# Performance work log

Hardware: AMD Instinct MI355X
Metric: run time of the kernel (lower is better)

The kernel has to match this reference:

```python
import jax, jax.numpy as jnp
import numpy as np

N_NODES = 100000
N_EDGES = 1600000
HEADS = 8
CH = 16
NEG_SLOPE = 0.2


def setup_inputs() -> dict:
    key = jax.random.key(0)
    ks = jax.random.split(key, 8)
    x = jax.random.normal(ks[0], (N_NODES, 16), dtype=jnp.float32)
    edge_index = jax.random.randint(ks[1], (2, N_EDGES), 0, N_NODES, dtype=jnp.int64)
    W = jax.random.normal(ks[2], (16, HEADS * CH), dtype=jnp.float32) * 0.25
    att_src = jax.random.normal(ks[3], (HEADS, CH), dtype=jnp.float32) * 0.25
    att_dst = jax.random.normal(ks[4], (HEADS, CH), dtype=jnp.float32) * 0.25
    bias = jax.random.normal(ks[5], (HEADS * CH,), dtype=jnp.float32) * 0.1
    fc_w = jax.random.normal(ks[6], (HEADS * CH, 5), dtype=jnp.float32) * 0.1
    fc_b = jax.random.normal(ks[7], (5,), dtype=jnp.float32) * 0.1
    return {"x": x, "edge_index": edge_index, "W": W, "att_src": att_src,
            "att_dst": att_dst, "bias": bias, "fc_w": fc_w, "fc_b": fc_b}


def reference(x, edge_index, W, att_src, att_dst, bias, fc_w, fc_b):
    N = x.shape[0]
    # PyG GATConv default: add self loops
    loops = jnp.arange(N, dtype=edge_index.dtype)
    src = jnp.concatenate([edge_index[0], loops])
    dst = jnp.concatenate([edge_index[1], loops])

    h = (x @ W).reshape(N, HEADS, CH)                 # [N,H,C]
    a_src = jnp.einsum('nhc,hc->nh', h, att_src)      # [N,H]
    a_dst = jnp.einsum('nhc,hc->nh', h, att_dst)      # [N,H]

    e = a_src[src] + a_dst[dst]                       # [E,H]
    e = jax.nn.leaky_relu(e, NEG_SLOPE)
    # segment softmax over edges grouped by destination node
    e_max = jax.ops.segment_max(e, dst, num_segments=N)
    e_exp = jnp.exp(e - e_max[dst])
    denom = jax.ops.segment_sum(e_exp, dst, num_segments=N)
    alpha = e_exp / (denom[dst] + 1e-16)              # [E,H]

    msg = alpha[:, :, None] * h[src]                  # [E,H,C]
    out = jax.ops.segment_sum(msg, dst, num_segments=N)  # [N,H,C]
    out = out.reshape(N, HEADS * CH) + bias           # concat heads + bias

    out = jax.nn.relu(out)
    # dropout is identity in eval mode
    logits = out @ fc_w + fc_b                        # [N,5]
    return jax.nn.log_softmax(logits, axis=1)
```

## Files before the change

### kernel.cpp

```cpp
#include <hip/hip_runtime.h>
#include <hip/hip_bf16.h>
#include <math.h>

#define N_NODES 100000
#define N_EDGES 1600000
#define HEADS 8
#define HC 128
#define LOG2E 1.44269504f

#define DPB 64
#define NB 1563
#define NBP (NB + 1)
#define NCH 512
#define EPC (N_EDGES / NCH)
#define CAPS 2048
#define NA 196

__global__ __launch_bounds__(512) void k_prep(
    const float* __restrict__ x, const float* __restrict__ W,
    const float* __restrict__ att_s, const float* __restrict__ att_d,
    const int* __restrict__ ei,
    unsigned short* __restrict__ a_srcb, float* __restrict__ a_dst,
    uint4* __restrict__ x2b,
    int* __restrict__ offs, unsigned* __restrict__ stg) {
    __shared__ int smem[2048 + EPC];
    __shared__ int ws8[8];
    int t = threadIdx.x;
    if (blockIdx.x >= NCH) {
        float* sM = (float*)smem;
        if (t < 256) {
            int k = t >> 4, h2 = t & 15;
            const float* av = (h2 < 8) ? att_s : att_d;
            int h = h2 & 7;
            float s = 0.f;
#pragma unroll
            for (int c = 0; c < 16; ++c)
                s = fmaf(W[k * HC + h * 16 + c], av[h * 16 + c], s);
            sM[k * 16 + h2] = s * LOG2E;
        }
        __syncthreads();
        int node = (blockIdx.x - NCH) * 512 + t;
        if (node < N_NODES) {
            const float4* xr = (const float4*)(x + node * 16);
            float4 x0 = xr[0], x1 = xr[1], x2 = xr[2], x3 = xr[3];
            float xv[16] = {x0.x, x0.y, x0.z, x0.w, x1.x, x1.y, x1.z, x1.w,
                            x2.x, x2.y, x2.z, x2.w, x3.x, x3.y, x3.z, x3.w};
            union { uint4 u[2]; __hip_bfloat162 b[8]; } px;
#pragma unroll
            for (int k = 0; k < 8; ++k)
                px.b[k] = __float22bfloat162_rn(float2{xv[2 * k], xv[2 * k + 1]});
            x2b[node * 2] = px.u[0];
            x2b[node * 2 + 1] = px.u[1];
#pragma unroll
            for (int h2 = 0; h2 < 16; ++h2) {
                float o = 0.f;
#pragma unroll
                for (int k = 0; k < 16; ++k) o = fmaf(xv[k], sM[k * 16 + h2], o);
                if (h2 < 8) a_srcb[node * 8 + h2] =
                    __bfloat16_as_ushort(__float2bfloat16(o));
                else        a_dst[node * 8 + (h2 - 8)] = o;
            }
        }
    } else {
        int* hist = smem;
        unsigned* entries = (unsigned*)(smem + 2048);
        int c = blockIdx.x;
        hist[t] = 0; hist[t + 512] = 0; hist[t + 1024] = 0; hist[t + 1536] = 0;
        __syncthreads();
        int beg = c * EPC, end = beg + EPC;
        for (int e = beg + t; e < end; e += 512)
            atomicAdd(&hist[ei[N_EDGES + e] >> 6], 1);
        __syncthreads();
        int i0 = 4 * t;
        int v0 = hist[i0], v1 = hist[i0 + 1], v2 = hist[i0 + 2], v3 = hist[i0 + 3];
        int s1 = v0 + v1, s2 = s1 + v2, T = s2 + v3;
        int lane = t & 63, wv = t >> 6;
        int inc = T;
#pragma unroll
        for (int off = 1; off < 64; off <<= 1) {
            int y = __shfl_up(inc, off);
            if (lane >= off) inc += y;
        }
        if (lane == 63) ws8[wv] = inc;
        __syncthreads();
        int wbase = 0;
        for (int k = 0; k < wv; ++k) wbase += ws8[k];
        int e0 = wbase + inc - T;
        hist[i0] = e0; hist[i0 + 1] = e0 + v0;
        hist[i0 + 2] = e0 + s1; hist[i0 + 3] = e0 + s2;
        __syncthreads();
        int row = c * NBP;
        for (int b = t; b < NB; b += 512) offs[row + b] = hist[b];
        if (t == 0) offs[row + NB] = EPC;
        __syncthreads();
        for (int e = beg + t; e < end; e += 512) {
            int src = ei[e], dst = ei[N_EDGES + e];
            int pos = atomicAdd(&hist[dst >> 6], 1);
            entries[pos] = ((unsigned)(dst & 63) << 17) | (unsigned)src;
        }
        __syncthreads();
        unsigned* so = stg + beg;
        for (int i = t; i < EPC; i += 512) so[i] = entries[i];
    }
}

__global__ __launch_bounds__(256) void k_tr(const int* __restrict__ offs,
                                            int* __restrict__ offsT) {
    __shared__ int tile[64][65];
    int b0 = (blockIdx.x >> 3) * 64;
    int c0 = (blockIdx.x & 7) * 64;
    int t = threadIdx.x;
    for (int i = t; i < 4096; i += 256) {
        int cc = i >> 6, bb = i & 63;
        int b = b0 + bb;
        tile[bb][cc] = (b < NBP) ? offs[(c0 + cc) * NBP + b] : 0;
    }
    __syncthreads();
    for (int i = t; i < 4096; i += 256) {
        int bb = i >> 6, cc = i & 63;
        int b = b0 + bb;
        if (b < NBP) offsT[b * NCH + c0 + cc] = tile[bb][cc];
    }
}

__global__ __launch_bounds__(512) void k_gather(
    const __hip_bfloat162* __restrict__ x2b,
    const unsigned short* __restrict__ a_srcb, const float* __restrict__ W,
    const float* __restrict__ a_dst,
    const int* __restrict__ offsT, const unsigned* __restrict__ stg,
    const float* __restrict__ bias, const float* __restrict__ fc_w,
    const float* __restrict__ fc_b, float* __restrict__ out) {
    __shared__ unsigned estage[CAPS];
    __shared__ int cstage[CAPS];
    __shared__ float sW[16 * HC];
    __shared__ int o0_s[NCH];
    __shared__ int myb_s[NCH + 1];
    __shared__ int hist[DPB];
    __shared__ int bs[DPB + 1];
    __shared__ int ws8[8];
    int b = blockIdx.x, t = threadIdx.x;
    int d0 = b * DPB;
    for (int i = t; i < 16 * HC; i += 512) sW[i] = W[i];
    int lane = t & 63, wv = t >> 6;
    {
        int o0 = offsT[b * NCH + t];
        int len = offsT[(b + 1) * NCH + t] - o0;
        o0_s[t] = o0;
        int inc = len;
#pragma unroll
        for (int off = 1; off < 64; off <<= 1) {
            int y = __shfl_up(inc, off);
            if (lane >= off) inc += y;
        }
        if (lane == 63) ws8[wv] = inc;
        __syncthreads();
        int wbase = 0;
        for (int k = 0; k < wv; ++k) wbase += ws8[k];
        myb_s[t] = wbase + inc - len;
        if (t == 511) myb_s[NCH] = wbase + inc;
    }
    if (t < DPB) hist[t] = (d0 + t < N_NODES) ? 1 : 0;
    __syncthreads();
    int tot = myb_s[NCH];
    for (int i = t; i < tot; i += 512) {
        int lo = 0, hi = NCH - 1;
#pragma unroll
        for (int s = 0; s < 9; ++s) {
            int mid = (lo + hi + 1) >> 1;
            if (myb_s[mid] <= i) lo = mid; else hi = mid - 1;
        }
        estage[i] = stg[lo * EPC + o0_s[lo] + (i - myb_s[lo])];
    }
    __syncthreads();
    for (int i = t; i < tot; i += 512) atomicAdd(&hist[estage[i] >> 17], 1);
    __syncthreads();
    if (t < 64) {
        int v = hist[t];
        int iv = v;
#pragma unroll
        for (int off = 1; off < 64; off <<= 1) {
            int y = __shfl_up(iv, off);
            if (t >= off) iv += y;
        }
        int excl = iv - v;
        bs[t] = excl;
        if (t == 63) bs[64] = iv;
        int gd = d0 + t;
        bool val = gd < N_NODES;
        if (val) cstage[excl] = gd;
        hist[t] = excl + (val ? 1 : 0);
    }
    __syncthreads();
    for (int i = t; i < tot; i += 512) {
        unsigned u = estage[i];
        int pos = atomicAdd(&hist[u >> 17], 1);
        cstage[pos] = (int)(u & 0x1FFFF);
    }
    __syncthreads();
    int q = t & 31, g = t >> 5;
    int head = q >> 2, i4 = q & 3;
    int c0 = q * 4;
    float b0 = bias[c0], b1 = bias[c0 + 1], b2 = bias[c0 + 2], b3 = bias[c0 + 3];
    float fw[4][5], fb[5];
#pragma unroll
    for (int k = 0; k < 4; ++k)
#pragma unroll
        for (int j = 0; j < 5; ++j) fw[k][j] = fc_w[(c0 + k) * 5 + j];
#pragma unroll
    for (int j = 0; j < 5; ++j) fb[j] = fc_b[j];
    for (int l4 = 0; l4 < 4; ++l4) {
        int l = g * 4 + l4;
        int gd = d0 + l;
        if (gd >= N_NODES) break;
        int beg = bs[l], end = bs[l + 1];
        float ad = a_dst[gd * 8 + head];
        float A0 = 0.f, A1 = 0.f, A2 = 0.f, A3 = 0.f, wsum = 0.f;
        int j = beg;
        for (; j + 2 <= end; j += 2) {
            int s0 = cstage[j], s1 = cstage[j + 1];
            unsigned short u0 = a_srcb[s0 * 8 + head];
            unsigned short u1 = a_srcb[s1 * 8 + head];
            union { uint2 u; __hip_bfloat162 bb[2]; } xa, xb;
            xa.u = *(const uint2*)(x2b + (size_t)s0 * 8 + i4 * 2);
            xb.u = *(const uint2*)(x2b + (size_t)s1 * 8 + i4 * 2);
            float e0 = __bfloat162float(__ushort_as_bfloat16(u0)) + ad;
            float e1 = __bfloat162float(__ushort_as_bfloat16(u1)) + ad;
            e0 = fmaxf(e0, 0.2f * e0);
            e1 = fmaxf(e1, 0.2f * e1);
            float w0 = exp2f(e0), w1 = exp2f(e1);
            float2 a01 = __bfloat1622float2(xa.bb[0]);
            float2 a23 = __bfloat1622float2(xa.bb[1]);
            float2 b01 = __bfloat1622float2(xb.bb[0]);
            float2 b23 = __bfloat1622float2(xb.bb[1]);
            A0 = fmaf(w0, a01.x, A0); A1 = fmaf(w0, a01.y, A1);
            A2 = fmaf(w0, a23.x, A2); A3 = fmaf(w0, a23.y, A3);
            A0 = fmaf(w1, b01.x, A0); A1 = fmaf(w1, b01.y, A1);
            A2 = fmaf(w1, b23.x, A2); A3 = fmaf(w1, b23.y, A3);
            wsum += w0 + w1;
        }
        if (j < end) {
            int s0 = cstage[j];
            float as = __bfloat162float(
                __ushort_as_bfloat16(a_srcb[s0 * 8 + head]));
            float e = as + ad;
            e = fmaxf(e, 0.2f * e);
            float w = exp2f(e);
            union { uint2 u; __hip_bfloat162 bb[2]; } xu;
            xu.u = *(const uint2*)(x2b + (size_t)s0 * 8 + i4 * 2);
            float2 f01 = __bfloat1622float2(xu.bb[0]);
            float2 f23 = __bfloat1622float2(xu.bb[1]);
            A0 = fmaf(w, f01.x, A0); A1 = fmaf(w, f01.y, A1);
            A2 = fmaf(w, f23.x, A2); A3 = fmaf(w, f23.y, A3);
            wsum += w;
        }
        float inv = 1.f / (wsum + 1e-16f);
        A0 *= inv; A1 *= inv; A2 *= inv; A3 *= inv;
        float ov0 = 0.f, ov1 = 0.f, ov2 = 0.f, ov3 = 0.f;
#pragma unroll
        for (int ii = 0; ii < 4; ++ii) {
            int sl = (q & 28) + ii;
            float a0 = __shfl(A0, sl, 32);
            float a1 = __shfl(A1, sl, 32);
            float a2 = __shfl(A2, sl, 32);
            float a3 = __shfl(A3, sl, 32);
            const float* w0 = sW + (4 * ii) * HC + c0;
            ov0 = fmaf(a0, w0[0], ov0); ov1 = fmaf(a0, w0[1], ov1);
            ov2 = fmaf(a0, w0[2], ov2); ov3 = fmaf(a0, w0[3], ov3);
            const float* w1 = w0 + HC;
            ov0 = fmaf(a1, w1[0], ov0); ov1 = fmaf(a1, w1[1], ov1);
            ov2 = fmaf(a1, w1[2], ov2); ov3 = fmaf(a1, w1[3], ov3);
            const float* w2 = w1 + HC;
            ov0 = fmaf(a2, w2[0], ov0); ov1 = fmaf(a2, w2[1], ov1);
            ov2 = fmaf(a2, w2[2], ov2); ov3 = fmaf(a2, w2[3], ov3);
            const float* w3 = w2 + HC;
            ov0 = fmaf(a3, w3[0], ov0); ov1 = fmaf(a3, w3[1], ov1);
            ov2 = fmaf(a3, w3[2], ov2); ov3 = fmaf(a3, w3[3], ov3);
        }
        ov0 = fmaxf(ov0 + b0, 0.f);
        ov1 = fmaxf(ov1 + b1, 0.f);
        ov2 = fmaxf(ov2 + b2, 0.f);
        ov3 = fmaxf(ov3 + b3, 0.f);
        float p[5];
#pragma unroll
        for (int j2 = 0; j2 < 5; ++j2)
            p[j2] = ov0 * fw[0][j2] + ov1 * fw[1][j2]
                  + ov2 * fw[2][j2] + ov3 * fw[3][j2];
#pragma unroll
        for (int off = 16; off >= 1; off >>= 1) {
#pragma unroll
            for (int j2 = 0; j2 < 5; ++j2) p[j2] += __shfl_xor(p[j2], off);
        }
        if (q == 0) {
            float lg[5], m = -1e30f;
#pragma unroll
            for (int j2 = 0; j2 < 5; ++j2) {
                lg[j2] = p[j2] + fb[j2];
                m = fmaxf(m, lg[j2]);
            }
            float sum = 0.f;
#pragma unroll
            for (int j2 = 0; j2 < 5; ++j2) sum += __expf(lg[j2] - m);
            float ls = m + __logf(sum);
#pragma unroll
            for (int j2 = 0; j2 < 5; ++j2) out[gd * 5 + j2] = lg[j2] - ls;
        }
    }
}

extern "C" void kernel_launch(void* const* d_in, const int* in_sizes, int n_in,
                              void* d_out, int out_size, void* d_ws, size_t ws_size,
                              hipStream_t stream) {
    const float* x     = (const float*)d_in[0];
    const int*   ei    = (const int*)d_in[1];
    const float* W     = (const float*)d_in[2];
    const float* att_s = (const float*)d_in[3];
    const float* att_d = (const float*)d_in[4];
    const float* bias  = (const float*)d_in[5];
    const float* fc_w  = (const float*)d_in[6];
    const float* fc_b  = (const float*)d_in[7];
    float* out = (float*)d_out;

    char* ws = (char*)d_ws;
    size_t off = 0;
    auto carve = [&](size_t bytes) {
        void* p = ws + off;
        off = (off + bytes + 255) & ~(size_t)255;
        return p;
    };
    unsigned short* a_srcb = (unsigned short*)carve((size_t)N_NODES * HEADS * 2);
    float*    a_dst = (float*)   carve((size_t)N_NODES * HEADS * 4);
    uint4*    x2b   = (uint4*)   carve((size_t)N_NODES * 32);
    int*      offs  = (int*)     carve((size_t)NCH * NBP * 4);
    int*      offsT = (int*)     carve((size_t)NBP * NCH * 4);
    unsigned* stg   = (unsigned*)carve((size_t)N_EDGES * 4);

    k_prep<<<NCH + NA, 512, 0, stream>>>(x, W, att_s, att_d, ei,
                                         a_srcb, a_dst, x2b, offs, stg);
    k_tr<<<200, 256, 0, stream>>>(offs, offsT);
    k_gather<<<NB, 512, 0, stream>>>((const __hip_bfloat162*)x2b, a_srcb, W,
                                     a_dst, offsT, stg, bias, fc_w, fc_b, out);
}
```

Measured before the change: 182.4 us.

## Restructure gather to one wavefront per node with edge-parallel lanes

Changes the per-node aggregation mapping. Before, a 32-lane half-wave handled one node with each lane owning 4 channels of one head. Now a full 64-lane wavefront handles each node: 8 lane groups stride over edges, each lane owns one head and loads the full 32-byte bf16 x row. Partial sums are combined with xor-shuffle reductions, and the W projection, bias and fc layers are read from staged shared memory. It also fuses the histogram atomic into the staging loop, removing one barrier and one pass. The aim is more memory-level parallelism per node with fewer redundant gathers, at the cost of more registers (16 accumulators) and heavier shuffle reductions.

```diff
diff --git a/kernel.cpp b/kernel.cpp
--- a/kernel.cpp
+++ b/kernel.cpp
@@ -133,6 +133,9 @@
     __shared__ unsigned estage[CAPS];
     __shared__ int cstage[CAPS];
     __shared__ float sW[16 * HC];
+    __shared__ float sad[DPB * 8];
+    __shared__ float sbias[HC];
+    __shared__ float sfc[HC * 5];
     __shared__ int o0_s[NCH];
     __shared__ int myb_s[NCH + 1];
     __shared__ int hist[DPB];
@@ -141,6 +144,12 @@
     int b = blockIdx.x, t = threadIdx.x;
     int d0 = b * DPB;
     for (int i = t; i < 16 * HC; i += 512) sW[i] = W[i];
+    if (t < HC) sbias[t] = bias[t];
+    for (int i = t; i < HC * 5; i += 512) sfc[i] = fc_w[i];
+    {
+        int gd = d0 + (t >> 3);
+        sad[t] = (gd < N_NODES) ? a_dst[gd * 8 + (t & 7)] : 0.f;
+    }
     int lane = t & 63, wv = t >> 6;
     {
         int o0 = offsT[b * NCH + t];
@@ -169,10 +178,10 @@
             int mid = (lo + hi + 1) >> 1;
             if (myb_s[mid] <= i) lo = mid; else hi = mid - 1;
         }
-        estage[i] = stg[lo * EPC + o0_s[lo] + (i - myb_s[lo])];
-    }
-    __syncthreads();
-    for (int i = t; i < tot; i += 512) atomicAdd(&hist[estage[i] >> 17], 1);
+        unsigned u = stg[lo * EPC + o0_s[lo] + (i - myb_s[lo])];
+        estage[i] = u;
+        atomicAdd(&hist[u >> 17], 1);
+    }
     __syncthreads();
     if (t < 64) {
         int v = hist[t];
@@ -197,110 +206,75 @@
         cstage[pos] = (int)(u & 0x1FFFF);
     }
     __syncthreads();
-    int q = t & 31, g = t >> 5;
-    int head = q >> 2, i4 = q & 3;
-    int c0 = q * 4;
-    float b0 = bias[c0], b1 = bias[c0 + 1], b2 = bias[c0 + 2], b3 = bias[c0 + 3];
-    float fw[4][5], fb[5];
-#pragma unroll
-    for (int k = 0; k < 4; ++k)
-#pragma unroll
-        for (int j = 0; j < 5; ++j) fw[k][j] = fc_w[(c0 + k) * 5 + j];
-#pragma unroll
-    for (int j = 0; j < 5; ++j) fb[j] = fc_b[j];
-    for (int l4 = 0; l4 < 4; ++l4) {
-        int l = g * 4 + l4;
+    int o = lane >> 3, p = lane & 7;
+    for (int l = wv * 8; l < wv * 8 + 8; ++l) {
         int gd = d0 + l;
         if (gd >= N_NODES) break;
         int beg = bs[l], end = bs[l + 1];
-        float ad = a_dst[gd * 8 + head];
-        float A0 = 0.f, A1 = 0.f, A2 = 0.f, A3 = 0.f, wsum = 0.f;
-        int j = beg;
-        for (; j + 2 <= end; j += 2) {
-            int s0 = cstage[j], s1 = cstage[j + 1];
-            unsigned short u0 = a_srcb[s0 * 8 + head];
-            unsigned short u1 = a_srcb[s1 * 8 + head];
-            union { uint2 u; __hip_bfloat162 bb[2]; } xa, xb;
-            xa.u = *(const uint2*)(x2b + (size_t)s0 * 8 + i4 * 2);
-            xb.u = *(const uint2*)(x2b + (size_t)s1 * 8 + i4 * 2);
-            float e0 = __bfloat162float(__ushort_as_bfloat16(u0)) + ad;
-            float e1 = __bfloat162float(__ushort_as_bfloat16(u1)) + ad;
-            e0 = fmaxf(e0, 0.2f * e0);
-            e1 = fmaxf(e1, 0.2f * e1);
-            float w0 = exp2f(e0), w1 = exp2f(e1);
-            float2 a01 = __bfloat1622float2(xa.bb[0]);
-            float2 a23 = __bfloat1622float2(xa.bb[1]);
-            float2 b01 = __bfloat1622float2(xb.bb[0]);
-            float2 b23 = __bfloat1622float2(xb.bb[1]);
-            A0 = fmaf(w0, a01.x, A0); A1 = fmaf(w0, a01.y, A1);
-            A2 = fmaf(w0, a23.x, A2); A3 = fmaf(w0, a23.y, A3);
-            A0 = fmaf(w1, b01.x, A0); A1 = fmaf(w1, b01.y, A1);
-            A2 = fmaf(w1, b23.x, A2); A3 = fmaf(w1, b23.y, A3);
-            wsum += w0 + w1;
-        }
-        if (j < end) {
-            int s0 = cstage[j];
+        float ad = sad[l * 8 + p];
+        float A[16];
+#pragma unroll
+        for (int k = 0; k < 16; ++k) A[k] = 0.f;
+        float wsum = 0.f;
+        for (int j = beg + o; j < end; j += 8) {
+            int src = cstage[j];
             float as = __bfloat162float(
-                __ushort_as_bfloat16(a_srcb[s0 * 8 + head]));
+                __ushort_as_bfloat16(a_srcb[src * 8 + p]));
             float e = as + ad;
             e = fmaxf(e, 0.2f * e);
             float w = exp2f(e);
-            union { uint2 u; __hip_bfloat162 bb[2]; } xu;
-            xu.u = *(const uint2*)(x2b + (size_t)s0 * 8 + i4 * 2);
-            float2 f01 = __bfloat1622float2(xu.bb[0]);
-            float2 f23 = __bfloat1622float2(xu.bb[1]);
-            A0 = fmaf(w, f01.x, A0); A1 = fmaf(w, f01.y, A1);
-            A2 = fmaf(w, f23.x, A2); A3 = fmaf(w, f23.y, A3);
+            const uint4* xr = (const uint4*)x2b + (size_t)src * 2;
+            union { uint4 u; __hip_bfloat162 bb[4]; } q0, q1;
+            q0.u = xr[0]; q1.u = xr[1];
+#pragma unroll
+            for (int k = 0; k < 4; ++k) {
+                float2 f0 = __bfloat1622float2(q0.bb[k]);
+                float2 f1 = __bfloat1622float2(q1.bb[k]);
+                A[2 * k]     = fmaf(w, f0.x, A[2 * k]);
+                A[2 * k + 1] = fmaf(w, f0.y, A[2 * k + 1]);
+                A[8 + 2 * k]     = fmaf(w, f1.x, A[8 + 2 * k]);
+                A[8 + 2 * k + 1] = fmaf(w, f1.y, A[8 + 2 * k + 1]);
+            }
             wsum += w;
         }
+#pragma unroll
+        for (int m = 8; m <= 32; m <<= 1) {
+#pragma unroll
+            for (int k = 0; k < 16; ++k) A[k] += __shfl_xor(A[k], m);
+            wsum += __shfl_xor(wsum, m);
+        }
         float inv = 1.f / (wsum + 1e-16f);
-        A0 *= inv; A1 *= inv; A2 *= inv; A3 *= inv;
-        float ov0 = 0.f, ov1 = 0.f, ov2 = 0.f, ov3 = 0.f;
-#pragma unroll
-        for (int ii = 0; ii < 4; ++ii) {
-            int sl = (q & 28) + ii;
-            float a0 = __shfl(A0, sl, 32);
-            float a1 = __shfl(A1, sl, 32);
-            float a2 = __shfl(A2, sl, 32);
-            float a3 = __shfl(A3, sl, 32);
-            const float* w0 = sW + (4 * ii) * HC + c0;
-            ov0 = fmaf(a0, w0[0], ov0); ov1 = fmaf(a0, w0[1], ov1);
-            ov2 = fmaf(a0, w0[2], ov2); ov3 = fmaf(a0, w0[3], ov3);
-            const float* w1 = w0 + HC;
-            ov0 = fmaf(a1, w1[0], ov0); ov1 = fmaf(a1, w1[1], ov1);
-            ov2 = fmaf(a1, w1[2], ov2); ov3 = fmaf(a1, w1[3], ov3);
-            const float* w2 = w1 + HC;
-            ov0 = fmaf(a2, w2[0], ov0); ov1 = fmaf(a2, w2[1], ov1);
-            ov2 = fmaf(a2, w2[2], ov2); ov3 = fmaf(a2, w2[3], ov3);
-            const float* w3 = w2 + HC;
-            ov0 = fmaf(a3, w3[0], ov0); ov1 = fmaf(a3, w3[1], ov1);
-            ov2 = fmaf(a3, w3[2], ov2); ov3 = fmaf(a3, w3[3], ov3);
-        }
-        ov0 = fmaxf(ov0 + b0, 0.f);
-        ov1 = fmaxf(ov1 + b1, 0.f);
-        ov2 = fmaxf(ov2 + b2, 0.f);
-        ov3 = fmaxf(ov3 + b3, 0.f);
-        float p[5];
+#pragma unroll
+        for (int k = 0; k < 16; ++k) A[k] *= inv;
+        int c0 = p * 16 + o * 2;
+        float ov0 = 0.f, ov1 = 0.f;
+#pragma unroll
+        for (int k = 0; k < 16; ++k) {
+            ov0 = fmaf(A[k], sW[k * HC + c0], ov0);
+            ov1 = fmaf(A[k], sW[k * HC + c0 + 1], ov1);
+        }
+        ov0 = fmaxf(ov0 + sbias[c0], 0.f);
+        ov1 = fmaxf(ov1 + sbias[c0 + 1], 0.f);
+        float pj[5];
 #pragma unroll
         for (int j2 = 0; j2 < 5; ++j2)
-            p[j2] = ov0 * fw[0][j2] + ov1 * fw[1][j2]
-                  + ov2 * fw[2][j2] + ov3 * fw[3][j2];
-#pragma unroll
-        for (int off = 16; off >= 1; off >>= 1) {
-#pragma unroll
-            for (int j2 = 0; j2 < 5; ++j2) p[j2] += __shfl_xor(p[j2], off);
-        }
-        if (q == 0) {
-            float lg[5], m = -1e30f;
+            pj[j2] = ov0 * sfc[c0 * 5 + j2] + ov1 * sfc[(c0 + 1) * 5 + j2];
+#pragma unroll
+        for (int m = 1; m < 64; m <<= 1) {
+#pragma unroll
+            for (int j2 = 0; j2 < 5; ++j2) pj[j2] += __shfl_xor(pj[j2], m);
+        }
+        if (lane == 0) {
+            float lg[5], mx = -1e30f;
 #pragma unroll
             for (int j2 = 0; j2 < 5; ++j2) {
-                lg[j2] = p[j2] + fb[j2];
-                m = fmaxf(m, lg[j2]);
+                lg[j2] = pj[j2] + fc_b[j2];
+                mx = fmaxf(mx, lg[j2]);
             }
             float sum = 0.f;
 #pragma unroll
-            for (int j2 = 0; j2 < 5; ++j2) sum += __expf(lg[j2] - m);
-            float ls = m + __logf(sum);
+            for (int j2 = 0; j2 < 5; ++j2) sum += __expf(lg[j2] - mx);
+            float ls = mx + __logf(sum);
 #pragma unroll
             for (int j2 = 0; j2 < 5; ++j2) out[gd * 5 + j2] = lg[j2] - ls;
         }
```

Result: slower. 261.7 us (+43.5%).
